# Optimization experiments

Hardware: AMD Instinct MI355X
Metric: run time of the kernel (lower is better)

The kernel has to match this reference:

```python
import jax, jax.numpy as jnp
import numpy as np

DIM = 1024
STATE = 256
B, S = 4, 4096

def setup_inputs() -> dict:
    key = jax.random.key(0)
    ks = jax.random.split(key, 8)
    sc_b = 1.0 / np.sqrt(DIM)
    sc_c = 1.0 / np.sqrt(STATE)
    return {
        "x": jax.random.normal(ks[0], (B, S, DIM), dtype=jnp.float32),
        "A": jax.random.normal(ks[1], (STATE,), dtype=jnp.float32) * 0.02,
        "B_w": jax.random.uniform(ks[2], (STATE, DIM), minval=-sc_b, maxval=sc_b),
        "B_b": jax.random.uniform(ks[3], (STATE,), minval=-sc_b, maxval=sc_b),
        "C_w": jax.random.uniform(ks[4], (DIM, STATE), minval=-sc_c, maxval=sc_c),
        "C_b": jax.random.uniform(ks[5], (DIM,), minval=-sc_c, maxval=sc_c),
        "D_w": jax.random.uniform(ks[6], (DIM, DIM), minval=-sc_b, maxval=sc_b),
        "D_b": jax.random.uniform(ks[7], (DIM,), minval=-sc_b, maxval=sc_b),
    }

def reference(x, A, B_w, B_b, C_w, C_b, D_w, D_b):
    # Precompute input projections in batch (the per-step loop only needs state*A + Bu)
    Bu = jnp.einsum('bsd,nd->bsn', x, B_w) + B_b          # [B,S,STATE]
    Du = jnp.einsum('bsd,ed->bse', x, D_w) + D_b          # [B,S,DIM]
    Aexp = jnp.exp(A)[None, :]                             # [1,STATE]
    state0 = jnp.zeros((x.shape[0], A.shape[0]), dtype=x.dtype)

    def step(state, bu_t):
        state = jnp.tanh(state * Aexp + bu_t)
        return state, state

    _, states = jax.lax.scan(step, state0, jnp.swapaxes(Bu, 0, 1))  # [S,B,STATE]
    states = jnp.swapaxes(states, 0, 1)                              # [B,S,STATE]
    y = jnp.einsum('bsn,en->bse', states, C_w) + C_b + Du
    return y
```

## Files before the change

### kernel.cpp

```cpp
#include <hip/hip_runtime.h>
#include <hip/hip_bf16.h>

#define DIM 1024
#define STATE 256
#define BATCH 4
#define SEQ 4096
#define M_TOT (BATCH * SEQ)

typedef short short8 __attribute__((ext_vector_type(8)));
typedef float f32x4 __attribute__((ext_vector_type(4)));

__device__ __forceinline__ unsigned short f2bf(float f) {
  unsigned int u = __float_as_uint(f);
  u += 0x7fff + ((u >> 16) & 1);
  return (unsigned short)(u >> 16);
}

__device__ __forceinline__ float bf2f(unsigned short u) {
  return __uint_as_float((unsigned int)u << 16);
}

__device__ __forceinline__ void gl_lds16(const void* g, void* l) {
  __builtin_amdgcn_global_load_lds(
      (const __attribute__((address_space(1))) void*)g,
      (__attribute__((address_space(3))) void*)l, 16, 0, 0);
}

#define C2F 2.8853900817779268f
#define LOG2EF 1.4426950408889634f
#define VMC(N) asm volatile("s_waitcnt vmcnt(" #N ")" ::: "memory")

__global__ __launch_bounds__(256) void convert_w(
    const float* __restrict__ Bw, const float* __restrict__ Cw,
    const float* __restrict__ Dw, unsigned short* __restrict__ bwb,
    unsigned short* __restrict__ wob) {
  const int bx = blockIdx.x;
  const int t = threadIdx.x;
  if (bx < 256) {
    const int c = t * 4;
    const float4 v = *(const float4*)(Bw + (size_t)bx * DIM + c);
    *(ushort4*)(bwb + (size_t)bx * DIM + c) =
        make_ushort4(f2bf(v.x), f2bf(v.y), f2bf(v.z), f2bf(v.w));
  } else {
    const int e0 = (bx - 256) * 4;
#pragma unroll
    for (int rr = 0; rr < 4; ++rr) {
      const int e = e0 + rr;
      if (t < 64) {
        const float4 v = *(const float4*)(Cw + (size_t)e * STATE + t * 4);
        *(ushort4*)(wob + (size_t)e * 1280 + t * 4) =
            make_ushort4(f2bf(v.x), f2bf(v.y), f2bf(v.z), f2bf(v.w));
      }
      const float4 v = *(const float4*)(Dw + (size_t)e * DIM + t * 4);
      *(ushort4*)(wob + (size_t)e * 1280 + 256 + t * 4) =
          make_ushort4(f2bf(v.x), f2bf(v.y), f2bf(v.z), f2bf(v.w));
    }
  }
}

__global__ __launch_bounds__(256, 2) void gemm_GX(
    const float* __restrict__ x,
    const unsigned short* __restrict__ bwb,
    const float* __restrict__ Bb,
    const float* __restrict__ A,
    unsigned short* __restrict__ G,
    unsigned short* __restrict__ xb)
{
  __shared__ char lds[81920];

  const int tid = threadIdx.x;
  const int wave = tid >> 6;
  const int lane = tid & 63;
  const int lr = lane & 15;
  const int lk = lane >> 4;
  const int m0 = blockIdx.x * 32;

  f32x4 acc[2][4];
#pragma unroll
  for (int i = 0; i < 2; ++i)
#pragma unroll
    for (int j = 0; j < 4; ++j) acc[i][j] = (f32x4){0.f, 0.f, 0.f, 0.f};

  const char* xB  = (const char*)x;
  const char* bwB = (const char*)bwb;
  char* xbB = (char*)xb;

  auto stage = [&](int kt) {
    if (kt >= 16) return;
    char* slot = lds + (kt & 1) * 40960;
#pragma unroll
    for (int i = 0; i < 2; ++i) {
      const int s = i * 256 + tid;
      const int r = s >> 4;
      const int c = (s & 15) ^ (r & 7);
      gl_lds16(xB + (size_t)(m0 + r) * 4096 + (size_t)kt * 256 + c * 16,
               slot + i * 4096 + wave * 1024);
    }
#pragma unroll
    for (int i = 0; i < 8; ++i) {
      const int s = i * 256 + tid;
      const int r = s >> 3;
      const int c = (s & 7) ^ (r & 7);
      gl_lds16(bwB + (size_t)r * 2048 + (size_t)kt * 128 + c * 16,
               slot + 8192 + i * 4096 + wave * 1024);
    }
  };

  stage(0);
  VMC(0);
  __builtin_amdgcn_s_barrier();
  stage(1);

  for (int t = 0; t < 16; ++t) {
    const char* As = lds + (t & 1) * 40960;
    const char* Bs = As + 8192;

    short8 af[2][2];
#pragma unroll
    for (int kk = 0; kk < 2; ++kk)
#pragma unroll
      for (int f = 0; f < 2; ++f) {
        const int row = f * 16 + lr;
        const int sw = row & 7;
        const f32x4 a0 = *(const f32x4*)(As + row * 256 + (((kk * 8 + 2 * lk)     ^ sw) << 4));
        const f32x4 a1 = *(const f32x4*)(As + row * 256 + (((kk * 8 + 2 * lk + 1) ^ sw) << 4));
        short8 v;
#pragma unroll
        for (int j = 0; j < 4; ++j) {
          v[j]     = (short)f2bf(a0[j]);
          v[4 + j] = (short)f2bf(a1[j]);
        }
        af[kk][f] = v;
      }

    if ((t & 3) == wave) {
#pragma unroll
      for (int kk = 0; kk < 2; ++kk)
#pragma unroll
        for (int f = 0; f < 2; ++f) {
          const int row = f * 16 + lr;
          *(short8*)(xbB + (size_t)(m0 + row) * 2048 +
                     (size_t)t * 128 + kk * 64 + lk * 16) = af[kk][f];
        }
    }

    short8 bfr[2][4];
#pragma unroll
    for (int kk = 0; kk < 2; ++kk)
#pragma unroll
      for (int fj = 0; fj < 4; ++fj) {
        const int n = wave * 64 + fj * 16 + lr;
        bfr[kk][fj] = *(const short8*)(Bs + n * 128 + (((kk * 4 + lk) ^ (n & 7)) << 4));
      }
#pragma unroll
    for (int kk = 0; kk < 2; ++kk)
#pragma unroll
      for (int f = 0; f < 2; ++f)
#pragma unroll
        for (int fj = 0; fj < 4; ++fj)
          acc[f][fj] = __builtin_amdgcn_mfma_f32_16x16x32_bf16(
              af[kk][f], bfr[kk][fj], acc[f][fj], 0, 0, 0);

    if (t < 15) {
      VMC(0);
      __builtin_amdgcn_s_barrier();
      stage(t + 2);
    }
  }

#pragma unroll
  for (int fj = 0; fj < 4; ++fj) {
    const int cg = wave * 64 + fj * 16 + lr;
    const float bbv = fmaf(Bb[cg], C2F,
                           C2F * __builtin_amdgcn_exp2f(A[cg] * LOG2EF));
#pragma unroll
    for (int f = 0; f < 2; ++f)
#pragma unroll
      for (int j = 0; j < 4; ++j) {
        const int rg = m0 + f * 16 + lk * 4 + j;
        G[(size_t)rg * STATE + cg] = f2bf(fmaf(acc[f][fj][j], C2F, bbv));
      }
  }
}

#define PH(TILE, Q, STG, VMST)                                                 \
  do {                                                                         \
    const char* As = lds + ((TILE) & 1) * 32768;                               \
    const char* Bs = lds + 65536 + ((TILE) & 1) * 32768;                       \
    if ((Q) == 0) {                                                            \
      _Pragma("unroll") for (int fj = 0; fj < 4; ++fj) {                       \
        const int r = wn * 64 + fj * 16 + lr;                                  \
        _Pragma("unroll") for (int kk = 0; kk < 2; ++kk)                       \
          bfr[fj][kk] = *(const short8*)(Bs + r * 128 +                        \
                                         (((kk * 4 + lk) ^ (r & 7)) << 4));    \
      }                                                                        \
    }                                                                          \
    short8 af[2][2];                                                           \
    _Pragma("unroll") for (int fl = 0; fl < 2; ++fl) {                         \
      const int r = wm * 128 + (Q) * 32 + fl * 16 + lr;                        \
      _Pragma("unroll") for (int kk = 0; kk < 2; ++kk)                         \
        af[fl][kk] = *(const short8*)(As + r * 128 +                           \
                                      (((kk * 4 + lk) ^ (r & 7)) << 4));       \
    }                                                                          \
    STG;                                                                       \
    if ((Q) == 0) asm volatile("s_waitcnt lgkmcnt(8)" ::: "memory");           \
    __builtin_amdgcn_s_barrier();                                              \
    __builtin_amdgcn_s_setprio(1);                                             \
    _Pragma("unroll") for (int kk = 0; kk < 2; ++kk)                           \
      _Pragma("unroll") for (int fl = 0; fl < 2; ++fl)                         \
        _Pragma("unroll") for (int fj = 0; fj < 4; ++fj)                       \
          acc[(Q) * 2 + fl][fj] = __builtin_amdgcn_mfma_f32_16x16x32_bf16(     \
              af[fl][kk], bfr[fj][kk], acc[(Q) * 2 + fl][fj], 0, 0, 0);        \
    __builtin_amdgcn_s_setprio(0);                                             \
    VMST;                                                                      \
    __builtin_amdgcn_s_barrier();                                              \
  } while (0)

__global__ __launch_bounds__(512, 2) void gemm_out(
    const unsigned short* __restrict__ G,
    unsigned short* __restrict__ stb,
    const unsigned short* __restrict__ xb,
    const unsigned short* __restrict__ wob,
    const float* __restrict__ Aarr,
    const float* __restrict__ Cb,
    const float* __restrict__ Db,
    float* __restrict__ dout)
{
  __shared__ char lds[131072];

  const int tid = threadIdx.x;
  const int wave = tid >> 6;
  const int lane = tid & 63;
  const int lr = lane & 15;
  const int lk = lane >> 4;
  const int wm = wave >> 2;
  const int wn = wave & 3;

  const int bs = ((blockIdx.x & 7) << 5) | (blockIdx.x >> 3);
  const int m0 = (bs >> 2) * 256;
  const int n0 = (bs & 3) * 256;

  {
    const int c2 = tid >> 8;
    const int n  = tid & 255;
    const int T0 = m0 & 4095;
    const int startT = (c2 == 0) ? ((T0 == 0) ? 0 : T0 - 64) : T0 + 64;
    const int nw = (c2 == 0 && T0 == 0) ? 0 : 64;
    const int total = nw + 128;
    const int mstart = (m0 - T0) + startT;
    const unsigned short* g = G + (size_t)mstart * STATE + n;
    unsigned short* q = stb + (size_t)mstart * STATE + n;
    const float P = C2F * __builtin_amdgcn_exp2f(Aarr[n] * LOG2EF);
    const float mP2 = -2.0f * P;

    float r = 0.5f;
    constexpr int CH = 16;
    float cur[CH], nxt[CH];
#pragma unroll
    for (int j = 0; j < CH; ++j) cur[j] = bf2f(g[(size_t)j * STATE]);

    const int NC = total / CH;
    for (int c = 0; c < NC; ++c) {
      if (c + 1 < NC) {
        const unsigned short* pn = g + (size_t)(c + 1) * CH * STATE;
#pragma unroll
        for (int j = 0; j < CH; ++j) nxt[j] = bf2f(pn[(size_t)j * STATE]);
      }
      if (c * CH >= nw) {
        unsigned short* qc = q + (size_t)c * CH * STATE;
#pragma unroll
        for (int j = 0; j < CH; ++j) {
          const float t = fmaf(mP2, r, cur[j]);
          const float e = __builtin_amdgcn_exp2f(t);
          r = __builtin_amdgcn_rcpf(1.0f + e);
          const float s = fmaf(-2.0f, r, 1.0f);
          qc[(size_t)j * STATE] = f2bf(s);
        }
      } else {
#pragma unroll
        for (int j = 0; j < CH; ++j) {
          const float t = fmaf(mP2, r, cur[j]);
          const float e = __builtin_amdgcn_exp2f(t);
          r = __builtin_amdgcn_rcpf(1.0f + e);
        }
      }
      if (c + 1 < NC) {
#pragma unroll
        for (int j = 0; j < CH; ++j) cur[j] = nxt[j];
      }
    }
  }
  VMC(0);
  __builtin_amdgcn_s_barrier();

  const char* stbB = (const char*)stb;
  const char* xbB  = (const char*)xb;
  const char* wobB = (const char*)wob;

  f32x4 acc[8][4];
#pragma unroll
  for (int i = 0; i < 8; ++i)
#pragma unroll
    for (int j = 0; j < 4; ++j) acc[i][j] = (f32x4){0.f, 0.f, 0.f, 0.f};

  auto stageA = [&](int kt, int h) {
    if (kt >= 20) return;
    const char* base;
    size_t str;
    size_t colb;
    if (kt < 4) { base = stbB; str = 512;  colb = (size_t)kt * 128; }
    else        { base = xbB;  str = 2048; colb = (size_t)(kt - 4) * 128; }
    base += (size_t)m0 * str;
#pragma unroll
    for (int i2 = 0; i2 < 2; ++i2) {
      const int s = i2 * 512 + tid;
      const int r = s >> 3;
      const int cl = (s & 7) ^ (r & 7);
      gl_lds16(base + (size_t)(h * 128 + r) * str + colb + cl * 16,
               lds + ((kt & 1) * 32768) + h * 16384 + i2 * 8192 + wave * 1024);
    }
  };
  auto stageB = [&](int kt, int h) {
    if (kt >= 20) return;
#pragma unroll
    for (int i2 = 0; i2 < 2; ++i2) {
      const int s = i2 * 512 + tid;
      const int r = s >> 3;
      const int cl = (s & 7) ^ (r & 7);
      gl_lds16(wobB + (size_t)(n0 + h * 128 + r) * 2560 + (size_t)kt * 128 + cl * 16,
               lds + 65536 + ((kt & 1) * 32768) + h * 16384 + i2 * 8192 + wave * 1024);
    }
  };

  stageA(0, 0); stageA(0, 1);
  stageB(0, 0); stageB(0, 1);
  stageB(1, 0); stageB(1, 1);
  VMC(4);
  __builtin_amdgcn_s_barrier();

  short8 bfr[4][2];
  for (int i = 0; i < 10; ++i) {
    const int e = 2 * i, o = e + 1;
    PH(e, 0, stageA(o, 0), );
    PH(e, 1, stageA(o, 1), );
    PH(e, 2, stageB(e + 2, 0), );
    PH(e, 3, stageB(e + 2, 1), if (i == 9) { VMC(0); } else { VMC(4); });
    PH(o, 0, stageA(e + 2, 0), );
    PH(o, 1, stageA(e + 2, 1), );
    PH(o, 2, stageB(o + 2, 0), );
    PH(o, 3, stageB(o + 2, 1), VMC(4));
  }

#pragma unroll
  for (int fj = 0; fj < 4; ++fj) {
    const int col = n0 + wn * 64 + fj * 16 + lr;
    const float cb = Cb[col] + Db[col];
#pragma unroll
    for (int m = 0; m < 8; ++m) {
      const int rowb = m0 + wm * 128 + m * 16 + lk * 4;
#pragma unroll
      for (int j = 0; j < 4; ++j)
        dout[(size_t)(rowb + j) * DIM + col] = acc[m][fj][j] + cb;
    }
  }
}

extern "C" void kernel_launch(void* const* d_in, const int* in_sizes, int n_in,
                              void* d_out, int out_size, void* d_ws, size_t ws_size,
                              hipStream_t stream) {
  const float* x  = (const float*)d_in[0];
  const float* A  = (const float*)d_in[1];
  const float* Bw = (const float*)d_in[2];
  const float* Bb = (const float*)d_in[3];
  const float* Cw = (const float*)d_in[4];
  const float* Cb = (const float*)d_in[5];
  const float* Dw = (const float*)d_in[6];
  const float* Db = (const float*)d_in[7];
  float* dout = (float*)d_out;

  char* ws = (char*)d_ws;
  unsigned short* xb   = (unsigned short*)(ws);
  unsigned short* bwb  = (unsigned short*)(ws + 33554432);
  unsigned short* wob  = (unsigned short*)(ws + 34078720);
  unsigned short* G    = (unsigned short*)(ws + 36700160);
  unsigned short* stb  = (unsigned short*)(ws + 53477376);

  convert_w<<<512, 256, 0, stream>>>(Bw, Cw, Dw, bwb, wob);
  gemm_GX<<<512, 256, 0, stream>>>(x, bwb, Bb, A, G, xb);
  gemm_out<<<256, 512, 0, stream>>>(G, stb, xb, wob, A, Cb, Db, dout);
}
```

Measured before the change: 89.46 us.

## Interleave two scan chains per thread and overlap with GEMM prologue loads

The in-block recurrence now has each thread run two independent 64-step chunks, each with its own warm-up, interleaved step by step. This halves the serial dependency length and hides exp/rcp latency through instruction-level parallelism. The fused GEMM K-loop is reordered to process the x/D columns first and the state columns last, so the first tile loads can be issued before the scan runs. The cost is more redundant warm-up computation, more registers, and a reordered K sequence that must stay in sync with the weight layout.

```diff
diff --git a/kernel.cpp b/kernel.cpp
--- a/kernel.cpp
+++ b/kernel.cpp
@@ -240,76 +240,17 @@
   const int m0 = (bs >> 2) * 256;
   const int n0 = (bs & 3) * 256;
 
-  {
-    const int c2 = tid >> 8;
-    const int n  = tid & 255;
-    const int T0 = m0 & 4095;
-    const int startT = (c2 == 0) ? ((T0 == 0) ? 0 : T0 - 64) : T0 + 64;
-    const int nw = (c2 == 0 && T0 == 0) ? 0 : 64;
-    const int total = nw + 128;
-    const int mstart = (m0 - T0) + startT;
-    const unsigned short* g = G + (size_t)mstart * STATE + n;
-    unsigned short* q = stb + (size_t)mstart * STATE + n;
-    const float P = C2F * __builtin_amdgcn_exp2f(Aarr[n] * LOG2EF);
-    const float mP2 = -2.0f * P;
-
-    float r = 0.5f;
-    constexpr int CH = 16;
-    float cur[CH], nxt[CH];
-#pragma unroll
-    for (int j = 0; j < CH; ++j) cur[j] = bf2f(g[(size_t)j * STATE]);
-
-    const int NC = total / CH;
-    for (int c = 0; c < NC; ++c) {
-      if (c + 1 < NC) {
-        const unsigned short* pn = g + (size_t)(c + 1) * CH * STATE;
-#pragma unroll
-        for (int j = 0; j < CH; ++j) nxt[j] = bf2f(pn[(size_t)j * STATE]);
-      }
-      if (c * CH >= nw) {
-        unsigned short* qc = q + (size_t)c * CH * STATE;
-#pragma unroll
-        for (int j = 0; j < CH; ++j) {
-          const float t = fmaf(mP2, r, cur[j]);
-          const float e = __builtin_amdgcn_exp2f(t);
-          r = __builtin_amdgcn_rcpf(1.0f + e);
-          const float s = fmaf(-2.0f, r, 1.0f);
-          qc[(size_t)j * STATE] = f2bf(s);
-        }
-      } else {
-#pragma unroll
-        for (int j = 0; j < CH; ++j) {
-          const float t = fmaf(mP2, r, cur[j]);
-          const float e = __builtin_amdgcn_exp2f(t);
-          r = __builtin_amdgcn_rcpf(1.0f + e);
-        }
-      }
-      if (c + 1 < NC) {
-#pragma unroll
-        for (int j = 0; j < CH; ++j) cur[j] = nxt[j];
-      }
-    }
-  }
-  VMC(0);
-  __builtin_amdgcn_s_barrier();
-
   const char* stbB = (const char*)stb;
   const char* xbB  = (const char*)xb;
   const char* wobB = (const char*)wob;
 
-  f32x4 acc[8][4];
-#pragma unroll
-  for (int i = 0; i < 8; ++i)
-#pragma unroll
-    for (int j = 0; j < 4; ++j) acc[i][j] = (f32x4){0.f, 0.f, 0.f, 0.f};
-
-  auto stageA = [&](int kt, int h) {
-    if (kt >= 20) return;
+  auto stageA = [&](int t, int h) {
+    if (t >= 20) return;
     const char* base;
     size_t str;
     size_t colb;
-    if (kt < 4) { base = stbB; str = 512;  colb = (size_t)kt * 128; }
-    else        { base = xbB;  str = 2048; colb = (size_t)(kt - 4) * 128; }
+    if (t < 16) { base = xbB;  str = 2048; colb = (size_t)t * 128; }
+    else        { base = stbB; str = 512;  colb = (size_t)(t - 16) * 128; }
     base += (size_t)m0 * str;
 #pragma unroll
     for (int i2 = 0; i2 < 2; ++i2) {
@@ -317,26 +258,99 @@
       const int r = s >> 3;
       const int cl = (s & 7) ^ (r & 7);
       gl_lds16(base + (size_t)(h * 128 + r) * str + colb + cl * 16,
-               lds + ((kt & 1) * 32768) + h * 16384 + i2 * 8192 + wave * 1024);
+               lds + ((t & 1) * 32768) + h * 16384 + i2 * 8192 + wave * 1024);
     }
   };
-  auto stageB = [&](int kt, int h) {
-    if (kt >= 20) return;
+  auto stageB = [&](int t, int h) {
+    if (t >= 20) return;
+    const int kt = (t < 16) ? t + 4 : t - 16;
 #pragma unroll
     for (int i2 = 0; i2 < 2; ++i2) {
       const int s = i2 * 512 + tid;
       const int r = s >> 3;
       const int cl = (s & 7) ^ (r & 7);
       gl_lds16(wobB + (size_t)(n0 + h * 128 + r) * 2560 + (size_t)kt * 128 + cl * 16,
-               lds + 65536 + ((kt & 1) * 32768) + h * 16384 + i2 * 8192 + wave * 1024);
+               lds + 65536 + ((t & 1) * 32768) + h * 16384 + i2 * 8192 + wave * 1024);
     }
   };
 
   stageA(0, 0); stageA(0, 1);
   stageB(0, 0); stageB(0, 1);
   stageB(1, 0); stageB(1, 1);
-  VMC(4);
+
+  {
+    const int s  = tid >> 8;
+    const int n  = tid & 255;
+    const int T0 = m0 & 4095;
+    const int nw0 = (T0 == 0 && s == 0) ? 0 : 64;
+    const int start0 = m0 + 64 * s - nw0;
+    const int start1 = m0 + 64 * s + 64;
+    const unsigned short* g0 = G + (size_t)start0 * STATE + n;
+    const unsigned short* g1 = G + (size_t)start1 * STATE + n;
+    unsigned short* q0 = stb + (size_t)start0 * STATE + n;
+    unsigned short* q1 = stb + (size_t)start1 * STATE + n;
+    const float P = C2F * __builtin_amdgcn_exp2f(Aarr[n] * LOG2EF);
+    const float mP2 = -2.0f * P;
+
+    float r0 = 0.5f, r1 = 0.5f;
+    constexpr int CH = 16;
+    const int NC0 = (nw0 + 64) / CH;
+    float cur0[CH], nxt0[CH], cur1[CH], nxt1[CH];
+#pragma unroll
+    for (int j = 0; j < CH; ++j) {
+      cur0[j] = bf2f(g0[(size_t)j * STATE]);
+      cur1[j] = bf2f(g1[(size_t)j * STATE]);
+    }
+
+    for (int c = 0; c < 8; ++c) {
+      const bool a0 = (c < NC0);
+      if (c + 1 < NC0) {
+        const unsigned short* p = g0 + (size_t)(c + 1) * CH * STATE;
+#pragma unroll
+        for (int j = 0; j < CH; ++j) nxt0[j] = bf2f(p[(size_t)j * STATE]);
+      }
+      if (c + 1 < 8) {
+        const unsigned short* p = g1 + (size_t)(c + 1) * CH * STATE;
+#pragma unroll
+        for (int j = 0; j < CH; ++j) nxt1[j] = bf2f(p[(size_t)j * STATE]);
+      }
+      const bool e0 = a0 && (c * CH >= nw0);
+      const bool e1 = (c >= 4);
+      unsigned short* qc0 = q0 + (size_t)c * CH * STATE;
+      unsigned short* qc1 = q1 + (size_t)c * CH * STATE;
+#pragma unroll
+      for (int j = 0; j < CH; ++j) {
+        if (a0) {
+          const float t0 = fmaf(mP2, r0, cur0[j]);
+          const float x0 = __builtin_amdgcn_exp2f(t0);
+          r0 = __builtin_amdgcn_rcpf(1.0f + x0);
+          if (e0) qc0[(size_t)j * STATE] = f2bf(fmaf(-2.0f, r0, 1.0f));
+        }
+        {
+          const float t1 = fmaf(mP2, r1, cur1[j]);
+          const float x1 = __builtin_amdgcn_exp2f(t1);
+          r1 = __builtin_amdgcn_rcpf(1.0f + x1);
+          if (e1) qc1[(size_t)j * STATE] = f2bf(fmaf(-2.0f, r1, 1.0f));
+        }
+      }
+      if (c + 1 < NC0) {
+#pragma unroll
+        for (int j = 0; j < CH; ++j) cur0[j] = nxt0[j];
+      }
+      if (c + 1 < 8) {
+#pragma unroll
+        for (int j = 0; j < CH; ++j) cur1[j] = nxt1[j];
+      }
+    }
+  }
+  VMC(0);
   __builtin_amdgcn_s_barrier();
+
+  f32x4 acc[8][4];
+#pragma unroll
+  for (int i = 0; i < 8; ++i)
+#pragma unroll
+    for (int j = 0; j < 4; ++j) acc[i][j] = (f32x4){0.f, 0.f, 0.f, 0.f};
 
   short8 bfr[4][2];
   for (int i = 0; i < 10; ++i) {
```

Measured after the change: 94.68 us. 1.06x slower.
